# Optimization experiments

Measured on AMD Instinct MI355X. Metric: run time of the kernel, lower is better.

The kernel has to match this reference:

```python
import jax, jax.numpy as jnp
import numpy as np

V, E, HD, T = 32000, 100, 256, 17   # vocab, embed dim, lstm hidden (bidir total), tagset
B, S = 64, 1024
H = HD // 2                         # per-direction hidden


def setup_inputs() -> dict:
    key = jax.random.key(0)
    ks = jax.random.split(key, 16)
    p = lambda k, sh: (jax.random.normal(k, sh, jnp.float32) * 0.1)
    sentence = jax.random.randint(ks[0], (B, S), 0, V)
    mask = jnp.ones((B, S), dtype=bool)
    embed = p(ks[1], (V, E)).at[0].set(0.0)  # padding_idx=0
    inp = {
        "sentence": sentence,
        "mask": mask,
        "embed": embed,
        "w_ih_f": p(ks[2], (4 * H, E)), "w_hh_f": p(ks[3], (4 * H, H)),
        "b_ih_f": p(ks[4], (4 * H,)), "b_hh_f": p(ks[5], (4 * H,)),
        "w_ih_b": p(ks[6], (4 * H, E)), "w_hh_b": p(ks[7], (4 * H, H)),
        "b_ih_b": p(ks[8], (4 * H,)), "b_hh_b": p(ks[9], (4 * H,)),
        "fc_w": p(ks[10], (T, HD)), "fc_b": p(ks[11], (T,)),
        "start_trans": p(ks[12], (T,)),
        "end_trans": p(ks[13], (T,)),
        "trans": p(ks[14], (T, T)),
    }
    return inp


def _lstm_dir(xs, w_ih, w_hh, b_ih, b_hh):
    # xs: [S, B, E] -> hs: [S, B, H]. PyTorch gate order: i, f, g, o.
    xg = jnp.einsum('sbe,ge->sbg', xs, w_ih) + b_ih  # precompute input projections
    h0 = jnp.zeros((xs.shape[1], H), xs.dtype)
    def step(carry, xg_t):
        h, c = carry
        g = xg_t + h @ w_hh.T + b_hh
        i, f, gg, o = jnp.split(g, 4, axis=-1)
        c = jax.nn.sigmoid(f) * c + jax.nn.sigmoid(i) * jnp.tanh(gg)
        h = jax.nn.sigmoid(o) * jnp.tanh(c)
        return (h, c), h
    _, hs = jax.lax.scan(step, (h0, h0), xg)
    return hs


def _emissions(sentence, embed, w_ih_f, w_hh_f, b_ih_f, b_hh_f,
               w_ih_b, w_hh_b, b_ih_b, b_hh_b, fc_w, fc_b):
    x = embed[sentence]                      # [B, S, E] (dropout is identity in eval)
    xs = x.transpose(1, 0, 2)                # [S, B, E]
    hf = _lstm_dir(xs, w_ih_f, w_hh_f, b_ih_f, b_hh_f)
    hb = _lstm_dir(xs[::-1], w_ih_b, w_hh_b, b_ih_b, b_hh_b)[::-1]
    hcat = jnp.concatenate([hf, hb], axis=-1)            # [S, B, 2H]
    return jnp.einsum('sbh,th->sbt', hcat, fc_w) + fc_b  # [S, B, T]


def reference(sentence, mask, embed, w_ih_f, w_hh_f, b_ih_f, b_hh_f,
              w_ih_b, w_hh_b, b_ih_b, b_hh_b, fc_w, fc_b,
              start_trans, end_trans, trans):
    em = _emissions(sentence, embed, w_ih_f, w_hh_f, b_ih_f, b_hh_f,
                    w_ih_b, w_hh_b, b_ih_b, b_hh_b, fc_w, fc_b)  # [S, B, T]
    mk = mask.T  # [S, B]

    # Viterbi forward pass (max-plus recurrence over the tagset)
    score0 = start_trans + em[0]  # [B, T]
    def vstep(score, inp):
        emit_t, mask_t = inp
        ns = score[:, :, None] + trans[None] + emit_t[:, None, :]  # [B, T_prev, T_cur]
        best = ns.max(axis=1)
        idx = jnp.argmax(ns, axis=1)                                # [B, T]
        score = jnp.where(mask_t[:, None], best, score)
        return score, idx
    score, hist = jax.lax.scan(vstep, score0, (em[1:], mk[1:]))    # hist: [S-1, B, T]
    score = score + end_trans
    last_tag = jnp.argmax(score, axis=-1)                          # [B]

    # Backtrace (mask-aware: frozen past sequence end)
    def back(tag, inp):
        idx_t, mask_t = inp
        prev = jnp.take_along_axis(idx_t, tag[:, None], axis=1)[:, 0]
        tag = jnp.where(mask_t, prev, tag)
        return tag, tag
    _, ys = jax.lax.scan(back, last_tag, (hist, mk[1:]), reverse=True)  # [S-1, B]
    path = jnp.concatenate([ys, last_tag[None]], axis=0).T              # [B, S]
    return path
```

## Files before the change

### kernel.cpp

```cpp
#include <hip/hip_runtime.h>
#include <math.h>

#define S_LEN 1024
#define BATCH 64
#define EDIM  100
#define HDIM  128
#define G4    512
#define TAGS  17
#define SGRP  15

typedef __attribute__((ext_vector_type(2))) float f32x2;
typedef __attribute__((ext_vector_type(4))) float f32x4;

__device__ __forceinline__ f32x2 pkfma(f32x2 a, f32x2 b, f32x2 c) {
    return __builtin_elementwise_fma(a, b, c);
}

template<int CTRL>
__device__ __forceinline__ float qperm(float x) {
    int i = __float_as_int(x);
    i = __builtin_amdgcn_update_dpp(0, i, CTRL, 0xF, 0xF, true);
    return __int_as_float(i);
}
#define QX1 qperm<0xB1>
#define QX2 qperm<0x4E>

__device__ __forceinline__ float fast_tanh_u(float x) {
    float e = __expf(-2.f * x);
    return fmaf(2.f, __builtin_amdgcn_rcpf(1.f + e), -1.f);
}

#define RDLANE(v, jj) __int_as_float(__builtin_amdgcn_readlane(__float_as_int(v), (jj)))

#define STEP_BARRIER() do {                                          \
    __builtin_amdgcn_sched_barrier(0);                               \
    asm volatile("s_waitcnt lgkmcnt(0)\n\ts_barrier" ::: "memory");  \
    __builtin_amdgcn_sched_barrier(0);                               \
} while (0)

__global__ __launch_bounds__(512, 1) void fused_scan_proj(
    const float* __restrict__ xgf_s, const float* __restrict__ xgb_s,
    const float* __restrict__ w_hh_f, const float* __restrict__ w_hh_b,
    float* __restrict__ hcat, float* __restrict__ h_state, float* __restrict__ c_state,
    int t0_scan, int clen, int nscan,
    const int* __restrict__ sentence, const float* __restrict__ embed,
    const float* __restrict__ w_ih_f, const float* __restrict__ b_ih_f, const float* __restrict__ b_hh_f,
    const float* __restrict__ w_ih_b, const float* __restrict__ b_ih_b, const float* __restrict__ b_hh_b,
    float* __restrict__ xgf_p, float* __restrict__ xgb_p, int t0_proj, int nproj_n,
    const float* __restrict__ fc_w, const float* __restrict__ fc_b,
    float* __restrict__ em, int fc_t0a, int fc_t0b)
{
    extern __shared__ float smem[];

    if ((int)blockIdx.x < nscan) {
        const int t     = threadIdx.x;
        const int gid   = t >> 2, q = t & 3;
        const int b     = blockIdx.x & 63;
        const int dir   = blockIdx.x >> 6;
        const int chain = blockIdx.x;

        const float* whh = dir ? w_hh_b : w_hh_f;
        f32x2 wl[4][8], wh[4][8];
#pragma unroll
        for (int g4 = 0; g4 < 4; ++g4) {
            const f32x4* wr = (const f32x4*)(whh + (g4 * HDIM + gid) * HDIM + q * 32);
#pragma unroll
            for (int i = 0; i < 8; ++i) {
                f32x4 v = wr[i];
                wl[g4][i] = v.xy;
                wh[g4][i] = v.zw;
            }
        }

        typedef float hl_t[4][36];
        hl_t* h_lds = (hl_t*)smem;
        float c_reg = 0.f;
        if (t0_scan == 0) {
            if (t < HDIM) h_lds[0][t >> 5][t & 31] = 0.f;
        } else {
            c_reg = c_state[chain * HDIM + gid];
            if (t < HDIM) h_lds[0][t >> 5][t & 31] = h_state[chain * HDIM + t];
        }
        __syncthreads();

        const float* xgp = (dir ? xgb_s : xgf_s) + (long)b * G4 + gid * 4;
        float4 z4; z4.x = z4.y = z4.z = z4.w = 0.f;
        float4 xgc = *(const float4*)xgp;
        float4 xgn = (clen > 1) ? *(const float4*)(xgp + (long)BATCH * G4) : z4;

        float* hc_base = hcat + (long)b * S_LEN * 256 + dir * HDIM + gid;
        float hv = 0.f;
        float hbuf[8];

        for (int sb = 0; sb < clen; sb += 8) {
#pragma unroll
            for (int k = 0; k < 8; ++k) {
                const int s = sb + k;
                float4 xg2 = z4;
                if (s + 2 < clen) xg2 = *(const float4*)(xgp + (long)(s + 2) * BATCH * G4);

                const int cur = k & 1;
                const float* hp = &h_lds[cur][q][0];
                f32x2 ac0 = {0.f, 0.f}, ac1 = {0.f, 0.f}, ac2 = {0.f, 0.f}, ac3 = {0.f, 0.f};
#pragma unroll
                for (int i = 0; i < 8; ++i) {
                    f32x4 h4 = *(const f32x4*)(hp + i * 4);
                    f32x2 hlo = h4.xy, hhi = h4.zw;
                    ac0 = pkfma(wl[0][i], hlo, ac0); ac0 = pkfma(wh[0][i], hhi, ac0);
                    ac1 = pkfma(wl[1][i], hlo, ac1); ac1 = pkfma(wh[1][i], hhi, ac1);
                    ac2 = pkfma(wl[2][i], hlo, ac2); ac2 = pkfma(wh[2][i], hhi, ac2);
                    ac3 = pkfma(wl[3][i], hlo, ac3); ac3 = pkfma(wh[3][i], hhi, ac3);
                }
                float a0 = ac0.x + ac0.y, a1 = ac1.x + ac1.y;
                float a2 = ac2.x + ac2.y, a3 = ac3.x + ac3.y;

                a0 += QX1(a0); a1 += QX1(a1); a2 += QX1(a2); a3 += QX1(a3);
                a0 += QX2(a0); a1 += QX2(a1); a2 += QX2(a2); a3 += QX2(a3);

                float av = (q == 0) ? a0 : (q == 1) ? a1 : (q == 2) ? a2 : a3;
                float xv = (q == 0) ? xgc.x : (q == 1) ? xgc.y : (q == 2) ? xgc.z : xgc.w;
                float pre = xv + av;
                float xin = (q == 2) ? 2.f * pre : pre;
                float e   = __expf(-xin);
                float sgm = __builtin_amdgcn_rcpf(1.f + e);
                float act = (q == 2) ? fmaf(2.f, sgm, -1.f) : sgm;
                float t1 = QX1(act);
                float t2 = QX2(act);
                float t3 = QX2(t1);
                float gi = (q == 0) ? act : (q == 1) ? t1 : (q == 2) ? t2 : t3;
                float gf = (q == 1) ? act : (q == 0) ? t1 : (q == 3) ? t2 : t3;
                float gg = (q == 2) ? act : (q == 3) ? t1 : (q == 0) ? t2 : t3;
                float go = (q == 3) ? act : (q == 2) ? t1 : (q == 1) ? t2 : t3;
                c_reg = gf * c_reg + gi * gg;
                hv = go * fast_tanh_u(c_reg);
                hbuf[k] = hv;

                if (q == 0) h_lds[cur ^ 1][gid >> 5][gid & 31] = hv;
                STEP_BARRIER();
                xgc = xgn; xgn = xg2;
            }
            if (q == 0) {
#pragma unroll
                for (int k = 0; k < 8; ++k) {
                    int tg = dir ? (S_LEN - 1 - (t0_scan + sb + k)) : (t0_scan + sb + k);
                    hc_base[(long)tg * 256] = hbuf[k];
                }
            }
        }

        if (q == 0) {
            c_state[chain * HDIM + gid] = c_reg;
            h_state[chain * HDIM + gid] = hv;
        }
    } else if ((int)blockIdx.x < nscan + nproj_n) {
        if (t0_proj < 0) return;
        const int pb   = blockIdx.x - nscan;
        const int tid  = threadIdx.x;
        const int row0 = pb * 16;

        float (*xf)[EDIM] = (float(*)[EDIM])smem;
        float (*xb)[EDIM] = (float(*)[EDIM])(smem + 1600);
        int* tok = (int*)(smem + 3200);

        if (tid < 32) {
            int r = tid & 15;
            int row = row0 + r;
            int s = row >> 6, b = row & 63;
            int tt = (tid < 16) ? (t0_proj + s) : (S_LEN - 1 - (t0_proj + s));
            tok[tid] = sentence[b * S_LEN + tt];
        }
        __syncthreads();
        for (int i = tid; i < 16 * EDIM; i += 512) {
            int r = i / EDIM, e = i - r * EDIM;
            xf[r][e] = embed[(long)tok[r] * EDIM + e];
            xb[r][e] = embed[(long)tok[16 + r] * EDIM + e];
        }
        __syncthreads();

        const float* wptr[2];
        float bias[2];
#pragma unroll
        for (int ci = 0; ci < 2; ++ci) {
            int c = tid + 512 * ci;
            if (c < G4) { wptr[ci] = w_ih_f + c * EDIM; bias[ci] = b_ih_f[c] + b_hh_f[c]; }
            else { int cb = c - G4; wptr[ci] = w_ih_b + cb * EDIM; bias[ci] = b_ih_b[cb] + b_hh_b[cb]; }
        }

        float acc[2][16];
#pragma unroll
        for (int ci = 0; ci < 2; ++ci)
#pragma unroll
            for (int r = 0; r < 16; ++r) acc[ci][r] = 0.f;

        for (int e = 0; e < EDIM; e += 4) {
            float4 w4[2];
#pragma unroll
            for (int ci = 0; ci < 2; ++ci) w4[ci] = *(const float4*)(wptr[ci] + e);
#pragma unroll
            for (int r = 0; r < 16; ++r) {
                float4 xvf = *(const float4*)&xf[r][e];
                float4 xvb = *(const float4*)&xb[r][e];
#pragma unroll
                for (int ci = 0; ci < 2; ++ci) {
                    float4 xv = (ci == 0) ? xvf : xvb;
                    acc[ci][r] = fmaf(w4[ci].x, xv.x, acc[ci][r]);
                    acc[ci][r] = fmaf(w4[ci].y, xv.y, acc[ci][r]);
                    acc[ci][r] = fmaf(w4[ci].z, xv.z, acc[ci][r]);
                    acc[ci][r] = fmaf(w4[ci].w, xv.w, acc[ci][r]);
                }
            }
        }

#pragma unroll
        for (int ci = 0; ci < 2; ++ci) {
            int c = tid + 512 * ci;
#pragma unroll
            for (int r = 0; r < 16; ++r) {
                int row = row0 + r;
                float v = acc[ci][r] + bias[ci];
                if (c < G4) xgf_p[(long)row * G4 + (c & 127) * 4 + (c >> 7)] = v;
                else { int cb = c - G4; xgb_p[(long)row * G4 + (cb & 127) * 4 + (cb >> 7)] = v; }
            }
        }
    } else {
        const int fcb0 = blockIdx.x - nscan - nproj_n;
        const int nfc1 = clen >> 1;
        int fb, ft0;
        if (fcb0 < nfc1) { fb = fcb0; ft0 = fc_t0a; }
        else             { fb = fcb0 - nfc1; ft0 = fc_t0b; }
        if (ft0 < 0) return;

        const int tid = threadIdx.x;
        float* w_lds = smem;
        float* part  = smem + TAGS * 256;

        for (int i = tid; i < TAGS * 256; i += 512) w_lds[i] = fc_w[i];
        __syncthreads();

        const int r = tid >> 2, p = tid & 3;
        const int idx0 = fb * 128 + r;
        const int b  = idx0 / clen;
        const int i0 = idx0 - b * clen;
        const long row = (long)b * S_LEN + ft0 + i0;
        const float* hrow = hcat + row * 256 + p * 64;

        float acc[TAGS];
#pragma unroll
        for (int tg = 0; tg < TAGS; ++tg) acc[tg] = 0.f;

        for (int e4 = 0; e4 < 16; ++e4) {
            float4 xv = *(const float4*)(hrow + e4 * 4);
            const float* wp = w_lds + p * 64 + e4 * 4;
#pragma unroll
            for (int tg = 0; tg < TAGS; ++tg) {
                acc[tg] = fmaf(xv.x, wp[tg * 256 + 0], acc[tg]);
                acc[tg] = fmaf(xv.y, wp[tg * 256 + 1], acc[tg]);
                acc[tg] = fmaf(xv.z, wp[tg * 256 + 2], acc[tg]);
                acc[tg] = fmaf(xv.w, wp[tg * 256 + 3], acc[tg]);
            }
        }
#pragma unroll
        for (int tg = 0; tg < TAGS; ++tg) part[(r * TAGS + tg) * 4 + p] = acc[tg];
        __syncthreads();

        for (int idx = tid; idx < 128 * TAGS; idx += 512) {
            int rr = idx / TAGS, tg = idx - rr * TAGS;
            const float* pp = part + (rr * TAGS + tg) * 4;
            float v = ((pp[0] + pp[1]) + (pp[2] + pp[3])) + fc_b[tg];
            int ridx = fb * 128 + rr;
            int bb = ridx / clen;
            int ii = ridx - bb * clen;
            em[((long)bb * S_LEN + ft0 + ii) * TAGS + tg] = v;
        }
    }
}

#define MAX3(a,b,c) fmaxf(fmaxf((a),(b)),(c))
#define MIN3(a,b,c) min(min((a),(b)),(c))

__device__ __forceinline__ float max17(const float* a) {
    float m0 = MAX3(a[0], a[1], a[2]);
    float m1 = MAX3(a[3], a[4], a[5]);
    float m2 = MAX3(a[6], a[7], a[8]);
    float m3 = MAX3(a[9], a[10], a[11]);
    float m4 = MAX3(a[12], a[13], a[14]);
    float m5 = fmaxf(a[15], a[16]);
    float n0 = MAX3(m0, m1, m2);
    float n1 = MAX3(m3, m4, m5);
    return fmaxf(n0, n1);
}

__global__ __launch_bounds__(64) void viterbi_score(
    const float* __restrict__ em,
    const float* __restrict__ start_trans, const float* __restrict__ end_trans,
    const float* __restrict__ trans,
    float* __restrict__ scores, int* __restrict__ last_tag)
{
    const int b = blockIdx.x;
    const int lane = threadIdx.x;
    __shared__ __align__(16) float e_lds[S_LEN * TAGS];

    {
        const float4* ef4 = (const float4*)(em + (long)b * S_LEN * TAGS);
        float4* el4 = (float4*)e_lds;
        for (int i = lane; i < (S_LEN * TAGS) / 4; i += 64) el4[i] = ef4[i];
    }
    const int cl = (lane < TAGS) ? lane : 0;
    float tcol[TAGS], etr[TAGS];
#pragma unroll
    for (int jj = 0; jj < TAGS; ++jj) {
        tcol[jj] = trans[jj * TAGS + cl];
        etr[jj]  = end_trans[jj];
    }
    __syncthreads();

    float sc = start_trans[cl] + e_lds[cl];
    float* sb = scores + (long)b * S_LEN * TAGS + cl;
    if (lane < TAGS) sb[0] = sc;

    float em_cur = e_lds[1 * TAGS + cl];
#pragma unroll 2
    for (int s = 1; s < S_LEN; ++s) {
        int sn = (s + 1 < S_LEN) ? (s + 1) : s;
        float em_next = e_lds[sn * TAGS + cl];

        float a[TAGS];
#pragma unroll
        for (int jj = 0; jj < TAGS; ++jj)
            a[jj] = RDLANE(sc, jj) + tcol[jj];

        float amax = max17(a);
        sc = amax + em_cur;
        if (lane < TAGS) sb[(long)s * TAGS] = sc;
        em_cur = em_next;
    }

    {
        float ev[TAGS];
#pragma unroll
        for (int jj = 0; jj < TAGS; ++jj) ev[jj] = RDLANE(sc, jj) + etr[jj];
        float bestv = max17(ev);
        int c[17];
#pragma unroll
        for (int j = 0; j < 17; ++j) c[j] = (ev[j] == bestv) ? j : 255;
        int m0 = MIN3(c[0], c[1], c[2]);
        int m1 = MIN3(c[3], c[4], c[5]);
        int m2 = MIN3(c[6], c[7], c[8]);
        int m3 = MIN3(c[9], c[10], c[11]);
        int m4 = MIN3(c[12], c[13], c[14]);
        int m5 = min(c[15], c[16]);
        int bt = min(MIN3(m0, m1, m2), MIN3(m3, m4, m5));
        if (lane == 0) last_tag[b] = bt;
    }
}

__global__ __launch_bounds__(256) void hist_kernel(
    const float* __restrict__ scores, const float* __restrict__ em,
    const float* __restrict__ trans, unsigned char* __restrict__ hist_g)
{
    const int nb = (S_LEN - 1 + SGRP - 1) / SGRP;
    const int b = blockIdx.x / nb, g = blockIdx.x % nb;
    const int t = threadIdx.x;
    __shared__ float s_sc[(SGRP + 1) * TAGS];
    __shared__ float s_em[(SGRP + 1) * TAGS];
    __shared__ float s_tr[TAGS * TAGS];

    const long b_base = (long)b * S_LEN * TAGS;
    const long maxoff = (long)S_LEN * TAGS - 1;
    for (int i = t; i < (SGRP + 1) * TAGS; i += 256) {
        long off = (long)g * SGRP * TAGS + i;
        long co  = off > maxoff ? maxoff : off;
        s_sc[i] = scores[b_base + co];
        s_em[i] = em[b_base + co];
    }
    for (int i = t; i < TAGS * TAGS; i += 256) s_tr[i] = trans[i];
    __syncthreads();

    if (t >= SGRP * TAGS) return;
    const int sl = t / TAGS, c = t - sl * TAGS;
    const int s = g * SGRP + sl + 1;
    if (s >= S_LEN) return;

    const float* sprev = s_sc + sl * TAGS;
    const float emv = s_em[(sl + 1) * TAGS + c];
    const float cur = s_sc[(sl + 1) * TAGS + c];

    int bi = 255;
#pragma unroll
    for (int j = TAGS - 1; j >= 0; --j) {
        float v = (sprev[j] + s_tr[j * TAGS + c]) + emv;
        if (v == cur) bi = j;
    }
    hist_g[((long)b * S_LEN + s) * TAGS + c] = (unsigned char)bi;
}

__global__ __launch_bounds__(64) void backtrace_kernel(
    const unsigned char* __restrict__ hist_g, const int* __restrict__ last_tag,
    int* __restrict__ out)
{
    const int b = blockIdx.x;
    const int lane = threadIdx.x;
    __shared__ int hist_i[(S_LEN * TAGS) / 4];
    __shared__ int tags[S_LEN];

    const int* hg = (const int*)(hist_g + (long)b * S_LEN * TAGS);
    for (int i = lane; i < (S_LEN * TAGS) / 4; i += 64) hist_i[i] = hg[i];
    __syncthreads();

    if (lane == 0) {
        const unsigned char* hl = (const unsigned char*)hist_i;
        int tag = last_tag[b];
        tags[S_LEN - 1] = tag;
        for (int s = S_LEN - 2; s >= 0; --s) {
            tag = hl[(s + 1) * TAGS + tag];
            tags[s] = tag;
        }
    }
    __syncthreads();
    for (int t = lane; t < S_LEN; t += 64) out[b * S_LEN + t] = tags[t];
}

extern "C" void kernel_launch(void* const* d_in, const int* in_sizes, int n_in,
                              void* d_out, int out_size, void* d_ws, size_t ws_size,
                              hipStream_t stream) {
    const int*   sentence    = (const int*)d_in[0];
    const float* embed       = (const float*)d_in[2];
    const float* w_ih_f      = (const float*)d_in[3];
    const float* w_hh_f      = (const float*)d_in[4];
    const float* b_ih_f      = (const float*)d_in[5];
    const float* b_hh_f      = (const float*)d_in[6];
    const float* w_ih_b      = (const float*)d_in[7];
    const float* w_hh_b      = (const float*)d_in[8];
    const float* b_ih_b      = (const float*)d_in[9];
    const float* b_hh_b      = (const float*)d_in[10];
    const float* fc_w        = (const float*)d_in[11];
    const float* fc_b        = (const float*)d_in[12];
    const float* start_trans = (const float*)d_in[13];
    const float* end_trans   = (const float*)d_in[14];
    const float* trans       = (const float*)d_in[15];
    int* out = (int*)d_out;

    const size_t hcat_e = (size_t)S_LEN * BATCH * 256;
    const size_t em_e   = (size_t)S_LEN * BATCH * TAGS;
    const size_t st_e   = (size_t)128 * HDIM;
    const size_t hist_e = (em_e + 3) / 4;
    const size_t fixed  = hcat_e + 2 * em_e + 2 * st_e + hist_e + 64;
    static const int cands[] = {1024, 512, 256, 128, 64};
    int C = 64;
    for (int ci = 0; ci < 5; ++ci) {
        int nch = S_LEN / cands[ci];
        size_t nbuf = (nch == 1) ? 2 : 4;
        size_t need = (nbuf * (size_t)cands[ci] * BATCH * G4 + fixed) * 4;
        if (need <= ws_size) { C = cands[ci]; break; }
    }
    const int nchunk = S_LEN / C;
    const size_t xg1 = (size_t)C * BATCH * G4;

    float* ws   = (float*)d_ws;
    float* xgf0 = ws;
    float* xgb0 = xgf0 + xg1;
    float* xgf1 = xgb0 + xg1;
    float* xgb1 = (nchunk > 1) ? xgf1 + xg1 : xgb0;
    float* base = (nchunk > 1) ? xgb1 + xg1 : xgf1;
    float* hcat     = base;
    float* em       = hcat + hcat_e;
    float* h_state  = em + em_e;
    float* c_state  = h_state + st_e;
    float* scores   = c_state + st_e;
    unsigned char* hist_g = (unsigned char*)(scores + em_e);
    int*   last_tag = (int*)(scores + em_e + hist_e);

    const int nproj = C * 4;
    const int nfc1  = C / 2;
    const size_t SM_SMALL = 3232 * sizeof(float);
    const size_t SM_FC    = 13056 * sizeof(float);

    fused_scan_proj<<<nproj, 512, SM_SMALL, stream>>>(
        nullptr, nullptr, w_hh_f, w_hh_b, hcat, h_state, c_state, 0, C, 0,
        sentence, embed, w_ih_f, b_ih_f, b_hh_f, w_ih_b, b_ih_b, b_hh_b,
        xgf0, xgb0, 0, nproj, fc_w, fc_b, em, -1, -1);

    for (int k = 0; k < nchunk; ++k) {
        const bool par1 = (k & 1) != 0;
        float* sf  = par1 ? xgf1 : xgf0;
        float* sbx = par1 ? xgb1 : xgb0;
        float* pf  = par1 ? xgf0 : xgf1;
        float* pbx = par1 ? xgb0 : xgb1;
        const bool hp = (k + 1 < nchunk);
        const int np = hp ? nproj : 0;

        int fca = -1, fcb = -1, nr = 0;
        if (2 * k >= nchunk + 1) {
            int m1 = k - 1, m2 = nchunk - k;
            fca = m1 * C; nr = 1;
            if (m2 != m1) { fcb = m2 * C; nr = 2; }
        }
        const int grid = 128 + np + nr * nfc1;
        const size_t sm = (nr > 0) ? SM_FC : SM_SMALL;
        fused_scan_proj<<<grid, 512, sm, stream>>>(
            sf, sbx, w_hh_f, w_hh_b, hcat, h_state, c_state, k * C, C, 128,
            sentence, embed, w_ih_f, b_ih_f, b_hh_f, w_ih_b, b_ih_b, b_hh_b,
            pf, pbx, hp ? (k + 1) * C : -1, np,
            fc_w, fc_b, em, fca, fcb);
    }
    {
        int fca = (nchunk - 1) * C;
        int fcb = (nchunk > 1) ? 0 : -1;
        int nr  = (nchunk > 1) ? 2 : 1;
        fused_scan_proj<<<nr * nfc1, 512, SM_FC, stream>>>(
            nullptr, nullptr, w_hh_f, w_hh_b, hcat, h_state, c_state, 0, C, 0,
            sentence, embed, w_ih_f, b_ih_f, b_hh_f, w_ih_b, b_ih_b, b_hh_b,
            nullptr, nullptr, -1, 0, fc_w, fc_b, em, fca, fcb);
    }

    viterbi_score<<<BATCH, 64, 0, stream>>>(
        em, start_trans, end_trans, trans, scores, last_tag);
    const int nb = (S_LEN - 1 + SGRP - 1) / SGRP;
    hist_kernel<<<BATCH * nb, 256, 0, stream>>>(scores, em, trans, hist_g);
    backtrace_kernel<<<BATCH, 64, 0, stream>>>(hist_g, last_tag, out);
}
```

Measured before the change: 1.088 ms.

## Fuse Viterbi score, history and backtrace into one LDS-resident decode kernel

Merges the three Viterbi kernels (forward scores, history recomputation, backtrace) into a single per-batch kernel that keeps scores, emissions and the backpointer table in LDS. This removes the global writes and reads of the score and history arrays and two kernel launches, and shrinks the workspace. It also raises wave priority for the LSTM scan blocks so they are favoured over co-resident projection blocks. In exchange, history computation now runs on only 64 blocks of 256 threads instead of a wide grid, and the kernel uses about 160KB of LDS per block.

```diff
diff --git a/kernel.cpp b/kernel.cpp
--- a/kernel.cpp
+++ b/kernel.cpp
@@ -7,7 +7,6 @@
 #define HDIM  128
 #define G4    512
 #define TAGS  17
-#define SGRP  15
 
 typedef __attribute__((ext_vector_type(2))) float f32x2;
 typedef __attribute__((ext_vector_type(4))) float f32x4;
@@ -53,6 +52,7 @@
     extern __shared__ float smem[];
 
     if ((int)blockIdx.x < nscan) {
+        __builtin_amdgcn_s_setprio(1);
         const int t     = threadIdx.x;
         const int gid   = t >> 2, q = t & 3;
         const int b     = blockIdx.x & 63;
@@ -152,6 +152,7 @@
             c_state[chain * HDIM + gid] = c_reg;
             h_state[chain * HDIM + gid] = hv;
         }
+        __builtin_amdgcn_s_setprio(0);
     } else if ((int)blockIdx.x < nscan + nproj_n) {
         if (t0_proj < 0) return;
         const int pb   = blockIdx.x - nscan;
@@ -290,52 +291,58 @@
     return fmaxf(n0, n1);
 }
 
-__global__ __launch_bounds__(64) void viterbi_score(
+__global__ __launch_bounds__(256) void decode_kernel(
     const float* __restrict__ em,
     const float* __restrict__ start_trans, const float* __restrict__ end_trans,
-    const float* __restrict__ trans,
-    float* __restrict__ scores, int* __restrict__ last_tag)
+    const float* __restrict__ trans, int* __restrict__ out)
 {
     const int b = blockIdx.x;
-    const int lane = threadIdx.x;
+    const int tid = threadIdx.x;
     __shared__ __align__(16) float e_lds[S_LEN * TAGS];
+    __shared__ __align__(16) float s_lds[S_LEN * TAGS];
+    __shared__ float s_tr[TAGS * TAGS];
+    __shared__ unsigned char hist[S_LEN * TAGS];
+    __shared__ int tags[S_LEN];
+    __shared__ int lt;
 
     {
         const float4* ef4 = (const float4*)(em + (long)b * S_LEN * TAGS);
         float4* el4 = (float4*)e_lds;
-        for (int i = lane; i < (S_LEN * TAGS) / 4; i += 64) el4[i] = ef4[i];
-    }
-    const int cl = (lane < TAGS) ? lane : 0;
-    float tcol[TAGS], etr[TAGS];
-#pragma unroll
-    for (int jj = 0; jj < TAGS; ++jj) {
-        tcol[jj] = trans[jj * TAGS + cl];
-        etr[jj]  = end_trans[jj];
+        for (int i = tid; i < (S_LEN * TAGS) / 4; i += 256) el4[i] = ef4[i];
+        for (int i = tid; i < TAGS * TAGS; i += 256) s_tr[i] = trans[i];
     }
     __syncthreads();
 
-    float sc = start_trans[cl] + e_lds[cl];
-    float* sb = scores + (long)b * S_LEN * TAGS + cl;
-    if (lane < TAGS) sb[0] = sc;
-
-    float em_cur = e_lds[1 * TAGS + cl];
+    if (tid < 64) {
+        const int lane = tid;
+        const int cl = (lane < TAGS) ? lane : 0;
+        float tcol[TAGS], etr[TAGS];
+#pragma unroll
+        for (int jj = 0; jj < TAGS; ++jj) {
+            tcol[jj] = s_tr[jj * TAGS + cl];
+            etr[jj]  = end_trans[jj];
+        }
+
+        float sc = start_trans[cl] + e_lds[cl];
+        if (lane < TAGS) s_lds[cl] = sc;
+
+        float em_cur = e_lds[1 * TAGS + cl];
 #pragma unroll 2
-    for (int s = 1; s < S_LEN; ++s) {
-        int sn = (s + 1 < S_LEN) ? (s + 1) : s;
-        float em_next = e_lds[sn * TAGS + cl];
-
-        float a[TAGS];
-#pragma unroll
-        for (int jj = 0; jj < TAGS; ++jj)
-            a[jj] = RDLANE(sc, jj) + tcol[jj];
-
-        float amax = max17(a);
-        sc = amax + em_cur;
-        if (lane < TAGS) sb[(long)s * TAGS] = sc;
-        em_cur = em_next;
-    }
-
-    {
+        for (int s = 1; s < S_LEN; ++s) {
+            int sn = (s + 1 < S_LEN) ? (s + 1) : s;
+            float em_next = e_lds[sn * TAGS + cl];
+
+            float a[TAGS];
+#pragma unroll
+            for (int jj = 0; jj < TAGS; ++jj)
+                a[jj] = RDLANE(sc, jj) + tcol[jj];
+
+            float amax = max17(a);
+            sc = amax + em_cur;
+            if (lane < TAGS) s_lds[s * TAGS + cl] = sc;
+            em_cur = em_next;
+        }
+
         float ev[TAGS];
 #pragma unroll
         for (int jj = 0; jj < TAGS; ++jj) ev[jj] = RDLANE(sc, jj) + etr[jj];
@@ -350,74 +357,36 @@
         int m4 = MIN3(c[12], c[13], c[14]);
         int m5 = min(c[15], c[16]);
         int bt = min(MIN3(m0, m1, m2), MIN3(m3, m4, m5));
-        if (lane == 0) last_tag[b] = bt;
-    }
-}
-
-__global__ __launch_bounds__(256) void hist_kernel(
-    const float* __restrict__ scores, const float* __restrict__ em,
-    const float* __restrict__ trans, unsigned char* __restrict__ hist_g)
-{
-    const int nb = (S_LEN - 1 + SGRP - 1) / SGRP;
-    const int b = blockIdx.x / nb, g = blockIdx.x % nb;
-    const int t = threadIdx.x;
-    __shared__ float s_sc[(SGRP + 1) * TAGS];
-    __shared__ float s_em[(SGRP + 1) * TAGS];
-    __shared__ float s_tr[TAGS * TAGS];
-
-    const long b_base = (long)b * S_LEN * TAGS;
-    const long maxoff = (long)S_LEN * TAGS - 1;
-    for (int i = t; i < (SGRP + 1) * TAGS; i += 256) {
-        long off = (long)g * SGRP * TAGS + i;
-        long co  = off > maxoff ? maxoff : off;
-        s_sc[i] = scores[b_base + co];
-        s_em[i] = em[b_base + co];
-    }
-    for (int i = t; i < TAGS * TAGS; i += 256) s_tr[i] = trans[i];
+        if (lane == 0) lt = bt;
+    }
     __syncthreads();
 
-    if (t >= SGRP * TAGS) return;
-    const int sl = t / TAGS, c = t - sl * TAGS;
-    const int s = g * SGRP + sl + 1;
-    if (s >= S_LEN) return;
-
-    const float* sprev = s_sc + sl * TAGS;
-    const float emv = s_em[(sl + 1) * TAGS + c];
-    const float cur = s_sc[(sl + 1) * TAGS + c];
-
-    int bi = 255;
-#pragma unroll
-    for (int j = TAGS - 1; j >= 0; --j) {
-        float v = (sprev[j] + s_tr[j * TAGS + c]) + emv;
-        if (v == cur) bi = j;
-    }
-    hist_g[((long)b * S_LEN + s) * TAGS + c] = (unsigned char)bi;
-}
-
-__global__ __launch_bounds__(64) void backtrace_kernel(
-    const unsigned char* __restrict__ hist_g, const int* __restrict__ last_tag,
-    int* __restrict__ out)
-{
-    const int b = blockIdx.x;
-    const int lane = threadIdx.x;
-    __shared__ int hist_i[(S_LEN * TAGS) / 4];
-    __shared__ int tags[S_LEN];
-
-    const int* hg = (const int*)(hist_g + (long)b * S_LEN * TAGS);
-    for (int i = lane; i < (S_LEN * TAGS) / 4; i += 64) hist_i[i] = hg[i];
+    for (int idx = tid; idx < (S_LEN - 1) * TAGS; idx += 256) {
+        int s = idx / TAGS + 1;
+        int c = idx - (s - 1) * TAGS;
+        const float* sprev = s_lds + (s - 1) * TAGS;
+        float emv = e_lds[s * TAGS + c];
+        float cur = s_lds[s * TAGS + c];
+        int bi = 255;
+#pragma unroll
+        for (int j = TAGS - 1; j >= 0; --j) {
+            float v = (sprev[j] + s_tr[j * TAGS + c]) + emv;
+            if (v == cur) bi = j;
+        }
+        hist[s * TAGS + c] = (unsigned char)bi;
+    }
     __syncthreads();
 
-    if (lane == 0) {
-        const unsigned char* hl = (const unsigned char*)hist_i;
-        int tag = last_tag[b];
+    if (tid == 0) {
+        int tag = lt;
         tags[S_LEN - 1] = tag;
         for (int s = S_LEN - 2; s >= 0; --s) {
-            tag = hl[(s + 1) * TAGS + tag];
+            tag = hist[(s + 1) * TAGS + tag];
             tags[s] = tag;
         }
     }
     __syncthreads();
-    for (int t = lane; t < S_LEN; t += 64) out[b * S_LEN + t] = tags[t];
+    for (int t = tid; t < S_LEN; t += 256) out[b * S_LEN + t] = tags[t];
 }
 
 extern "C" void kernel_launch(void* const* d_in, const int* in_sizes, int n_in,
@@ -443,8 +412,7 @@
     const size_t hcat_e = (size_t)S_LEN * BATCH * 256;
     const size_t em_e   = (size_t)S_LEN * BATCH * TAGS;
     const size_t st_e   = (size_t)128 * HDIM;
-    const size_t hist_e = (em_e + 3) / 4;
-    const size_t fixed  = hcat_e + 2 * em_e + 2 * st_e + hist_e + 64;
+    const size_t fixed  = hcat_e + em_e + 2 * st_e + 64;
     static const int cands[] = {1024, 512, 256, 128, 64};
     int C = 64;
     for (int ci = 0; ci < 5; ++ci) {
@@ -466,9 +434,6 @@
     float* em       = hcat + hcat_e;
     float* h_state  = em + em_e;
     float* c_state  = h_state + st_e;
-    float* scores   = c_state + st_e;
-    unsigned char* hist_g = (unsigned char*)(scores + em_e);
-    int*   last_tag = (int*)(scores + em_e + hist_e);
 
     const int nproj = C * 4;
     const int nfc1  = C / 2;
@@ -513,9 +478,6 @@
             nullptr, nullptr, -1, 0, fc_w, fc_b, em, fca, fcb);
     }
 
-    viterbi_score<<<BATCH, 64, 0, stream>>>(
-        em, start_trans, end_trans, trans, scores, last_tag);
-    const int nb = (S_LEN - 1 + SGRP - 1) / SGRP;
-    hist_kernel<<<BATCH * nb, 256, 0, stream>>>(scores, em, trans, hist_g);
-    backtrace_kernel<<<BATCH, 64, 0, stream>>>(hist_g, last_tag, out);
-}
+    decode_kernel<<<BATCH, 256, 0, stream>>>(
+        em, start_trans, end_trans, trans, out);
+}
```

After: 1.087 ms. No clear change (-0.1%).
